# Performance work log

Measured on AMD Instinct MI355X. Metric: run time of the kernel, lower is better.

The kernel has to match this reference:

```python
import jax, jax.numpy as jnp
import numpy as np

EPS = 1e-5

def _lstm_scan(x, mask, Wih, Whh, bih, bhh):
    # x: [B,T,D], mask: [B,T] float (applied to h and c AFTER each step, like the torch code)
    B, T, _ = x.shape
    H = Whh.shape[1]
    x_t = jnp.swapaxes(x, 0, 1)            # [T,B,D]
    m_t = jnp.swapaxes(mask, 0, 1)[:, :, None]  # [T,B,1]
    bias = bih + bhh
    def step(carry, inp):
        h, c = carry
        xt, mt = inp
        gates = xt @ Wih.T + h @ Whh.T + bias   # [B,4H], torch gate order i,f,g,o
        i, f, g, o = jnp.split(gates, 4, axis=-1)
        c = jax.nn.sigmoid(f) * c + jax.nn.sigmoid(i) * jnp.tanh(g)
        h = jax.nn.sigmoid(o) * jnp.tanh(c)
        h = h * mt
        c = c * mt
        return (h, c), h
    h0 = jnp.zeros((B, H), x.dtype)
    _, ys = jax.lax.scan(step, (h0, h0), (x_t, m_t))
    return jnp.swapaxes(ys, 0, 1)          # [B,T,H]

def _layernorm(x, g, b):
    mu = x.mean(-1, keepdims=True)
    var = ((x - mu) ** 2).mean(-1, keepdims=True)
    return (x - mu) * jax.lax.rsqrt(var + EPS) * g + b

def setup_inputs() -> dict:
    key = jax.random.key(0)
    ks = jax.random.split(key, 18)
    B, T, D, H, C = 64, 512, 256, 512, 1000
    def u(k, shape, fan):
        s = 1.0 / np.sqrt(fan)
        return jax.random.uniform(k, shape, jnp.float32, -s, s)
    x = jax.random.normal(ks[0], (B, T, D), jnp.float32)
    reset_mask = jax.random.randint(ks[1], (B, T), 0, 2).astype(jnp.float32)
    return {
        "x": x, "reset_mask": reset_mask,
        # layer 0 LSTM (torch init: U(-1/sqrt(H), 1/sqrt(H)))
        "Wih0": u(ks[2], (4 * H, D), H), "Whh0": u(ks[3], (4 * H, H), H),
        "bih0": u(ks[4], (4 * H,), H), "bhh0": u(ks[5], (4 * H,), H),
        "g0": jnp.ones((H,), jnp.float32), "beta0": jnp.zeros((H,), jnp.float32),
        # layer 1 LSTM
        "Wih1": u(ks[6], (4 * H, H), H), "Whh1": u(ks[7], (4 * H, H), H),
        "bih1": u(ks[8], (4 * H,), H), "bhh1": u(ks[9], (4 * H,), H),
        "g1": jnp.ones((H,), jnp.float32), "beta1": jnp.zeros((H,), jnp.float32),
        # final classifier
        "fcW": u(ks[10], (C, H), H), "fcb": u(ks[11], (C,), H),
    }

def reference(x, reset_mask, Wih0, Whh0, bih0, bhh0, g0, beta0,
              Wih1, Whh1, bih1, bhh1, g1, beta1, fcW, fcb):
    h = _lstm_scan(x, reset_mask, Wih0, Whh0, bih0, bhh0)
    h = _layernorm(jax.nn.relu(h), g0, beta0)
    h = _lstm_scan(h, reset_mask, Wih1, Whh1, bih1, bhh1)
    h = _layernorm(jax.nn.relu(h), g1, beta1)
    return h[:, -1, :] @ fcW.T + fcb        # [B, num_classes]
```

## Files before the change

kernel.cpp:

```cpp
#include <hip/hip_runtime.h>
#include <stdint.h>

#define BB 64
#define TT 512
#define DD 256
#define HH 512
#define NG 2048
#define BT (BB*TT)
#define NCLS 1000
#define MAXS 16

typedef _Float16 f16;
typedef _Float16 f16x2 __attribute__((ext_vector_type(2)));
typedef _Float16 f16x4 __attribute__((ext_vector_type(4)));
typedef _Float16 f16x8 __attribute__((ext_vector_type(8)));
typedef float f32x4 __attribute__((ext_vector_type(4)));

__device__ const int d_OFF[MAXS] = {0,32768,49152,60096,68288,74880,80384,85120,
                                    89216,92864,96192,99200,101952,104512,106880,109120};

__device__ __forceinline__ float sigf(float x) { return 1.0f / (1.0f + __expf(-x)); }
__device__ __forceinline__ float tanh_(float x) {
  float e = __expf(-2.0f * fabsf(x));
  float r = (1.0f - e) / (1.0f + e);
  return copysignf(r, x);
}
__device__ __forceinline__ f32x4 mfma16(f16x8 a, f16x8 b, f32x4 c) {
  return __builtin_amdgcn_mfma_f32_16x16x32_f16(a, b, c, 0, 0, 0);
}
__device__ __forceinline__ void gload16(const void* g, void* l) {
  __builtin_amdgcn_global_load_lds((const __attribute__((address_space(1))) void*)g,
                                   (__attribute__((address_space(3))) void*)l, 16, 0, 0);
}

#define C0 (NG*DD/4)
#define C1 (C0 + NG*HH/4)
#define C2 (C1 + NG*HH/4)
#define C3 (C2 + NG*HH/4)
#define CX (C3 + BT*DD/4)
__global__ __launch_bounds__(256) void prep_weights(
    const float* __restrict__ Wih0, const float* __restrict__ Whh0,
    const float* __restrict__ Wih1, const float* __restrict__ Whh1,
    const float* __restrict__ x,
    const float* __restrict__ bih0, const float* __restrict__ bhh0,
    const float* __restrict__ bih1, const float* __restrict__ bhh1,
    f16* __restrict__ W16ih0, f16* __restrict__ W16hh0,
    f16* __restrict__ W16ih1, f16* __restrict__ W16hh1,
    f16* __restrict__ AX,
    float* __restrict__ bias0, float* __restrict__ bias1) {
  int gi = blockIdx.x * 256 + threadIdx.x;
  for (int i = gi; i < CX; i += gridDim.x * 256) {
    const float* s; f16* d; int o;
    if (i < C0)      { s = Wih0; d = W16ih0; o = i; }
    else if (i < C1) { s = Whh0; d = W16hh0; o = i - C0; }
    else if (i < C2) { s = Wih1; d = W16ih1; o = i - C1; }
    else if (i < C3) { s = Whh1; d = W16hh1; o = i - C2; }
    else             { s = x;    d = AX;     o = i - C3; }
    float4 v = ((const float4*)s)[o];
    f16x4 h = { (f16)v.x, (f16)v.y, (f16)v.z, (f16)v.w };
    ((f16x4*)d)[o] = h;
  }
  if (gi < NG/2) {
    int j = gi * 2;
    bias0[j]   = bih0[j]   + bhh0[j];
    bias0[j+1] = bih0[j+1] + bhh0[j+1];
    bias1[j]   = bih1[j]   + bhh1[j];
    bias1[j+1] = bih1[j+1] + bhh1[j+1];
  }
}

__global__ __launch_bounds__(512) void build_lists(const float* __restrict__ mask,
    int* __restrict__ counts, int* __restrict__ lists,
    int* __restrict__ tailcnt, int* __restrict__ taillist,
    float* __restrict__ selm) {
  int b = blockIdx.x, t = threadIdx.x;
  __shared__ float sm[512];
  __shared__ int lcnt[MAXS], lbase[MAXS];
  sm[t] = mask[b*TT + t];
  if (t < MAXS) lcnt[t] = 0;
  __syncthreads();
  int run = 0;
  for (int j = 1; j <= MAXS; ++j) {
    if (t - j < 0) break;
    if (sm[t - j] != 0.0f) run++; else break;
  }
  selm[b*TT + t] = (run == 0) ? sm[t] : -1.0f;
  bool tail = (run >= MAXS);
  int slot = -1;
  if (!tail && run > 0) slot = atomicAdd(&lcnt[run], 1);
  __syncthreads();
  if (t < MAXS) lbase[t] = atomicAdd(&counts[t*32], lcnt[t]);
  __syncthreads();
  if (!tail && run > 0) lists[d_OFF[run] + lbase[run] + slot] = b*TT + t;
  unsigned long long bal = __ballot(tail);
  int lane = t & 63, w = t >> 6;
  int wpre = __popcll(bal & ((1ull << lane) - 1ull));
  __shared__ int wsum[8];
  if (lane == 0) wsum[w] = __popcll(bal);
  __syncthreads();
  int base = 0;
  for (int i = 0; i < w; ++i) base += wsum[i];
  if (tail) taillist[b*TT + base + wpre] = t;
  if (t == 0) {
    int tot = 0;
    for (int i = 0; i < 8; ++i) tot += wsum[i];
    tailcnt[b] = tot;
  }
}

__global__ __launch_bounds__(512) void proj_act(const f16* __restrict__ A,
    const f16* __restrict__ W, const float* __restrict__ bias,
    f16* __restrict__ G, f16* __restrict__ HS, f16* __restrict__ CS,
    const float* __restrict__ selm, int K) {
  __shared__ __align__(16) f16 smem[128*64 + 256*64];
  f16* As = smem;
  f16* Bs = smem + 128*64;
  __shared__ float sel[128];
  const int nwg = gridDim.x;
  const int cpx = nwg >> 3;
  const int swz = (blockIdx.x & 7) * cpx + (blockIdx.x >> 3);
  const int m0 = (swz >> 3) * 128;
  const int j0 = (swz & 7) * 64;
  const int tid = threadIdx.x;
  const int lane = tid & 63;
  const int w = tid >> 6;
  if (tid < 128) sel[tid] = selm[m0 + tid];

  const f16* asrc[2];
#pragma unroll
  for (int p = 0; p < 2; ++p) {
    int cid = tid + p*512;
    int r = cid >> 3, c = cid & 7;
    int cs = c ^ (r & 7);
    asrc[p] = A + (size_t)(m0 + r)*K + cs*8;
  }
  const f16* bsrc[4];
#pragma unroll
  for (int p = 0; p < 4; ++p) {
    int cid = tid + p*512;
    int grow = cid >> 3, c = cid & 7;
    int cs = c ^ (grow & 7);
    int wrow = (grow >> 6)*512 + j0 + (grow & 63);
    bsrc[p] = W + (size_t)wrow*K + cs*8;
  }

  const int rg = w >> 2;
  const int jg = w & 3;
  const int cl = lane & 15;
  const int kq = lane >> 4;
  f32x4 acc[4][4] = {};

  for (int k0 = 0; k0 < K; k0 += 64) {
#pragma unroll
    for (int p = 0; p < 2; ++p)
      gload16(asrc[p] + k0, As + (tid + p*512)*8);
#pragma unroll
    for (int p = 0; p < 4; ++p)
      gload16(bsrc[p] + k0, Bs + (tid + p*512)*8);
    __syncthreads();
#pragma unroll
    for (int ks = 0; ks < 2; ++ks) {
      int kc = ks*4 + kq;
      f16x8 af[4], bf[4];
#pragma unroll
      for (int mi = 0; mi < 4; ++mi) {
        int row = rg*64 + mi*16 + cl;
        af[mi] = *(const f16x8*)(As + row*64 + ((kc ^ (row & 7))*8));
      }
#pragma unroll
      for (int g = 0; g < 4; ++g) {
        int brow = g*64 + jg*16 + cl;
        bf[g] = *(const f16x8*)(Bs + brow*64 + ((kc ^ (brow & 7))*8));
      }
#pragma unroll
      for (int mi = 0; mi < 4; ++mi)
#pragma unroll
        for (int g = 0; g < 4; ++g)
          acc[mi][g] = mfma16(af[mi], bf[g], acc[mi][g]);
    }
    __syncthreads();
  }

  const int j = j0 + jg*16 + cl;
#pragma unroll
  for (int g = 0; g < 4; ++g) {
    float bb = bias[g*512 + j];
#pragma unroll
    for (int mi = 0; mi < 4; ++mi)
#pragma unroll
      for (int r = 0; r < 4; ++r)
        acc[mi][g][r] += bb;
  }

  f16* stg = smem;
#pragma unroll
  for (int half = 0; half < 2; ++half) {
    if (rg == half) {
#pragma unroll
      for (int mi = 0; mi < 4; ++mi)
#pragma unroll
        for (int g = 0; g < 4; ++g)
#pragma unroll
          for (int r = 0; r < 4; ++r) {
            int row_l = mi*16 + kq*4 + r;
            stg[row_l*264 + g*64 + jg*16 + cl] = (f16)acc[mi][g][r];
          }
    }
    __syncthreads();
    {
      int row_l = tid >> 3, sl = tid & 7;
      int slot = half*64 + row_l;
      int row = m0 + slot;
      int jj = j0 + sl*8;
      f16x8 vi = *(const f16x8*)(stg + row_l*264 +        sl*8);
      f16x8 vf = *(const f16x8*)(stg + row_l*264 +  64 + sl*8);
      f16x8 vg = *(const f16x8*)(stg + row_l*264 + 128 + sl*8);
      f16x8 vo = *(const f16x8*)(stg + row_l*264 + 192 + sl*8);
      float sm = sel[slot];
      if (sm >= 0.0f) {
        f16x8 hv, cv;
#pragma unroll
        for (int e = 0; e < 8; ++e) {
          float c = sigf((float)vi[e]) * tanh_((float)vg[e]);
          float h = sigf((float)vo[e]) * tanh_(c);
          hv[e] = (f16)(h*sm); cv[e] = (f16)(c*sm);
        }
        *(f16x8*)(HS + (size_t)row*HH + jj) = hv;
        *(f16x8*)(CS + (size_t)row*HH + jj) = cv;
      } else {
        *(f16x8*)(G + (size_t)row*NG +        jj) = vi;
        *(f16x8*)(G + (size_t)row*NG +  512 + jj) = vf;
        *(f16x8*)(G + (size_t)row*NG + 1024 + jj) = vg;
        *(f16x8*)(G + (size_t)row*NG + 1536 + jj) = vo;
      }
    }
    __syncthreads();
  }
}

__global__ __launch_bounds__(512) void lstm_step(const f16* __restrict__ Wh,
    const f16* __restrict__ G, f16* __restrict__ HS, f16* __restrict__ CS,
    const float* __restrict__ mask, const int* __restrict__ counts,
    const int* __restrict__ lists, int s) {
  const int cnt = counts[s*32];
  if (cnt == 0) return;
  const int units = ((cnt + 127) >> 7) * 8;
  const int* lst = lists + d_OFF[s];
  const int tid = threadIdx.x;
  const int lane = tid & 63;
  const int w = tid >> 6;
  __shared__ __align__(16) f16 smem[128*64 + 256*64];
  f16* As = smem;
  f16* Bs = smem + 128*64;
  __shared__ int ridx[128];
  __shared__ float rmk[128];
  const int rg = w >> 2;
  const int jg = w & 3;
  const int cl = lane & 15;
  const int kq = lane >> 4;

  for (int u = blockIdx.x; u < units; u += gridDim.x) {
    const int mbase = (u >> 3) * 128;
    const int j0 = (u & 7) * 64;
    if (tid < 128) {
      int i = mbase + tid;
      int r = (i < cnt) ? lst[i] : -1;
      ridx[tid] = r;
      rmk[tid] = (r >= 0) ? mask[r] : 0.0f;
    }
    __syncthreads();

    const f16* asrc[2];
#pragma unroll
    for (int p = 0; p < 2; ++p) {
      int cid = tid + p*512;
      int r = cid >> 3, c = cid & 7;
      int cs = c ^ (r & 7);
      int rr = ridx[r];
      int sr = (rr >= 1 ? rr : 1) - 1;
      asrc[p] = HS + (size_t)sr*HH + cs*8;
    }
    const f16* bsrc[4];
#pragma unroll
    for (int p = 0; p < 4; ++p) {
      int cid = tid + p*512;
      int grow = cid >> 3, c = cid & 7;
      int cs = c ^ (grow & 7);
      int wrow = (grow >> 6)*512 + j0 + (grow & 63);
      bsrc[p] = Wh + (size_t)wrow*HH + cs*8;
    }

    f32x4 acc[4][4] = {};
    for (int k0 = 0; k0 < HH; k0 += 64) {
#pragma unroll
      for (int p = 0; p < 2; ++p)
        gload16(asrc[p] + k0, As + (tid + p*512)*8);
#pragma unroll
      for (int p = 0; p < 4; ++p)
        gload16(bsrc[p] + k0, Bs + (tid + p*512)*8);
      __syncthreads();
#pragma unroll
      for (int ks = 0; ks < 2; ++ks) {
        int kc = ks*4 + kq;
        f16x8 af[4], bf[4];
#pragma unroll
        for (int mi = 0; mi < 4; ++mi) {
          int row = rg*64 + mi*16 + cl;
          af[mi] = *(const f16x8*)(As + row*64 + ((kc ^ (row & 7))*8));
        }
#pragma unroll
        for (int g = 0; g < 4; ++g) {
          int brow = g*64 + jg*16 + cl;
          bf[g] = *(const f16x8*)(Bs + brow*64 + ((kc ^ (brow & 7))*8));
        }
#pragma unroll
        for (int mi = 0; mi < 4; ++mi)
#pragma unroll
          for (int g = 0; g < 4; ++g)
            acc[mi][g] = mfma16(af[mi], bf[g], acc[mi][g]);
      }
      __syncthreads();
    }

    f16* stg = smem;
#pragma unroll
    for (int half = 0; half < 2; ++half) {
      if (rg == half) {
#pragma unroll
        for (int mi = 0; mi < 4; ++mi)
#pragma unroll
          for (int g = 0; g < 4; ++g)
#pragma unroll
            for (int r = 0; r < 4; ++r) {
              int row_l = mi*16 + kq*4 + r;
              stg[row_l*264 + g*64 + jg*16 + cl] = (f16)acc[mi][g][r];
            }
      }
      __syncthreads();
      {
        int row_l = tid >> 3, sl = tid & 7;
        int slot = half*64 + row_l;
        int row = ridx[slot];
        if (row >= 0) {
          int jj = j0 + sl*8;
          f16x8 ai = *(const f16x8*)(stg + row_l*264 +        sl*8);
          f16x8 af2 = *(const f16x8*)(stg + row_l*264 +  64 + sl*8);
          f16x8 ag = *(const f16x8*)(stg + row_l*264 + 128 + sl*8);
          f16x8 ao = *(const f16x8*)(stg + row_l*264 + 192 + sl*8);
          f16x8 Gi = *(const f16x8*)(G + (size_t)row*NG +        jj);
          f16x8 Gf = *(const f16x8*)(G + (size_t)row*NG +  512 + jj);
          f16x8 Gg = *(const f16x8*)(G + (size_t)row*NG + 1024 + jj);
          f16x8 Go = *(const f16x8*)(G + (size_t)row*NG + 1536 + jj);
          f16x8 cp = *(const f16x8*)(CS + (size_t)(row - 1)*HH + jj);
          float m = rmk[slot];
          f16x8 hv, cv;
#pragma unroll
          for (int e = 0; e < 8; ++e) {
            float gi = (float)ai[e] + (float)Gi[e];
            float gf = (float)af2[e] + (float)Gf[e];
            float gg = (float)ag[e] + (float)Gg[e];
            float go = (float)ao[e] + (float)Go[e];
            float c = sigf(gf)*(float)cp[e] + sigf(gi)*tanh_(gg);
            float h = sigf(go)*tanh_(c);
            hv[e] = (f16)(h*m); cv[e] = (f16)(c*m);
          }
          *(f16x8*)(HS + (size_t)row*HH + jj) = hv;
          *(f16x8*)(CS + (size_t)row*HH + jj) = cv;
        }
      }
      __syncthreads();
    }
  }
}

__global__ __launch_bounds__(512) void lstm_step_thin(const f16* __restrict__ Wh,
    const f16* __restrict__ G, f16* __restrict__ HS, f16* __restrict__ CS,
    const float* __restrict__ mask, const int* __restrict__ counts,
    const int* __restrict__ lists, int s) {
  const int cnt = counts[s*32];
  if (cnt == 0) return;
  const int units = ((cnt + 127) >> 7) * 32;
  const int* lst = lists + d_OFF[s];
  const int tid = threadIdx.x;
  const int lane = tid & 63;
  const int w = tid >> 6;
  __shared__ __align__(16) f16 As[128*64];
  __shared__ __align__(16) f16 Bs[64*64];
  __shared__ int ridx[128];
  __shared__ float rmk[128];
  const int cl = lane & 15;
  const int kq = lane >> 4;
  const int rbase = w * 16;

  for (int u = blockIdx.x; u < units; u += gridDim.x) {
    const int mbase = (u >> 5) * 128;
    const int j0 = (u & 31) * 16;
    if (tid < 128) {
      int i = mbase + tid;
      int r = (i < cnt) ? lst[i] : -1;
      ridx[tid] = r;
      rmk[tid] = (r >= 0) ? mask[r] : 0.0f;
    }
    __syncthreads();

    const f16* asrc[2];
#pragma unroll
    for (int p = 0; p < 2; ++p) {
      int cid = tid + p*512;
      int r = cid >> 3, c = cid & 7;
      int cs = c ^ (r & 7);
      int rr = ridx[r];
      int sr = (rr >= 1 ? rr : 1) - 1;
      asrc[p] = HS + (size_t)sr*HH + cs*8;
    }
    const f16* bsrc;
    {
      int grow = tid >> 3, c = tid & 7;
      int cs = c ^ (grow & 7);
      int wrow = (grow >> 4)*512 + j0 + (grow & 15);
      bsrc = Wh + (size_t)wrow*HH + cs*8;
    }

    f32x4 acc[4] = {};
    for (int k0 = 0; k0 < HH; k0 += 64) {
#pragma unroll
      for (int p = 0; p < 2; ++p)
        gload16(asrc[p] + k0, As + (tid + p*512)*8);
      gload16(bsrc + k0, Bs + tid*8);
      __syncthreads();
#pragma unroll
      for (int ks = 0; ks < 2; ++ks) {
        int kc = ks*4 + kq;
        int arow = rbase + cl;
        f16x8 af = *(const f16x8*)(As + arow*64 + ((kc ^ (arow & 7))*8));
        f16x8 bf[4];
#pragma unroll
        for (int g = 0; g < 4; ++g) {
          int brow = g*16 + cl;
          bf[g] = *(const f16x8*)(Bs + brow*64 + ((kc ^ (brow & 7))*8));
        }
#pragma unroll
        for (int g = 0; g < 4; ++g)
          acc[g] = mfma16(af, bf[g], acc[g]);
      }
      __syncthreads();
    }

    const int j = j0 + cl;
#pragma unroll
    for (int r = 0; r < 4; ++r) {
      int slot = rbase + kq*4 + r;
      int row = ridx[slot];
      if (row >= 0) {
        size_t gb = (size_t)row * NG;
        float gi = acc[0][r] + (float)G[gb + j];
        float gf = acc[1][r] + (float)G[gb + 512 + j];
        float gg = acc[2][r] + (float)G[gb + 1024 + j];
        float go = acc[3][r] + (float)G[gb + 1536 + j];
        float cp = (float)CS[(size_t)(row - 1)*HH + j];
        float c = sigf(gf)*cp + sigf(gi)*tanh_(gg);
        float h = sigf(go)*tanh_(c);
        float m = rmk[slot];
        HS[(size_t)row*HH + j] = (f16)(h*m);
        CS[(size_t)row*HH + j] = (f16)(c*m);
      }
    }
    __syncthreads();
  }
}

__global__ __launch_bounds__(512) void lstm_tail(const f16* __restrict__ Wh,
    const f16* __restrict__ G, f16* __restrict__ HS, f16* __restrict__ CS,
    const float* __restrict__ mask, const int* __restrict__ tailcnt,
    const int* __restrict__ taillist) {
  int b = blockIdx.x;
  int n = tailcnt[b];
  if (n == 0) return;
  int tid = threadIdx.x, lane = tid & 63, w = tid >> 6;
  const int rl = lane >> 3;
  const int kb = (lane & 7) * 8;
  __shared__ __align__(16) f16 hsh[HH];
  __shared__ float gsh[NG];
  for (int i = 0; i < n; ++i) {
    int t = taillist[b*TT + i];
    size_t row = (size_t)b*TT + t;
    if (tid < 256)
      ((uint32_t*)hsh)[tid] = ((const uint32_t*)(HS + (row - 1)*HH))[tid];
    __syncthreads();
    f16x8 hreg[8];
#pragma unroll
    for (int kk = 0; kk < 8; ++kk)
      hreg[kk] = *(const f16x8*)(hsh + kb + kk*64);
#pragma unroll 2
    for (int batch = 0; batch < 32; ++batch) {
      int o = (w*32 + batch)*8 + rl;
      const f16* wrow = Wh + (size_t)o*HH + kb;
      float p = 0.0f;
#pragma unroll
      for (int kk = 0; kk < 8; ++kk) {
        f16x8 wv = *(const f16x8*)(wrow + kk*64);
        f16x2 w0 = {wv[0], wv[1]}, w1 = {wv[2], wv[3]}, w2 = {wv[4], wv[5]}, w3 = {wv[6], wv[7]};
        f16x2 h0 = {hreg[kk][0], hreg[kk][1]}, h1 = {hreg[kk][2], hreg[kk][3]},
              h2 = {hreg[kk][4], hreg[kk][5]}, h3 = {hreg[kk][6], hreg[kk][7]};
        p = __builtin_amdgcn_fdot2(w0, h0, p, false);
        p = __builtin_amdgcn_fdot2(w1, h1, p, false);
        p = __builtin_amdgcn_fdot2(w2, h2, p, false);
        p = __builtin_amdgcn_fdot2(w3, h3, p, false);
      }
      p += __shfl_xor(p, 1);
      p += __shfl_xor(p, 2);
      p += __shfl_xor(p, 4);
      if ((lane & 7) == 0) gsh[o] = p + (float)G[row*NG + o];
    }
    __syncthreads();
    {
      float cp = (float)CS[(row - 1)*HH + tid];
      float c = sigf(gsh[512 + tid])*cp + sigf(gsh[tid])*tanh_(gsh[1024 + tid]);
      float h = sigf(gsh[1536 + tid])*tanh_(c);
      float m = mask[row];
      HS[row*HH + tid] = (f16)(h*m);
      CS[row*HH + tid] = (f16)(c*m);
    }
    __syncthreads();
  }
}

__global__ __launch_bounds__(512) void ln_relu(const f16* __restrict__ in,
    const float* __restrict__ g, const float* __restrict__ be,
    f16* __restrict__ out) {
  int lane = threadIdx.x & 63, w = threadIdx.x >> 6;
  int row = blockIdx.x * 8 + w;
  f16x8 hv = *(const f16x8*)(in + (size_t)row*HH + lane*8);
  float xv[8]; float s1 = 0.f, s2 = 0.f;
#pragma unroll
  for (int e = 0; e < 8; ++e) { float x = fmaxf((float)hv[e], 0.f); xv[e] = x; s1 += x; s2 += x*x; }
#pragma unroll
  for (int o = 1; o < 64; o <<= 1) { s1 += __shfl_xor(s1, o); s2 += __shfl_xor(s2, o); }
  float mu = s1 * (1.0f/512.0f);
  float var = s2 * (1.0f/512.0f) - mu*mu;
  float rs = rsqrtf(var + 1e-5f);
  f16x8 ov;
#pragma unroll
  for (int e = 0; e < 8; ++e) ov[e] = (f16)((xv[e] - mu)*rs*g[lane*8+e] + be[lane*8+e]);
  *(f16x8*)(out + (size_t)row*HH + lane*8) = ov;
}

__global__ __launch_bounds__(512) void ln_last(const f16* __restrict__ HS,
    const float* __restrict__ g, const float* __restrict__ be, float* __restrict__ out) {
  int b = blockIdx.x;
  int j = threadIdx.x;
  float x = fmaxf((float)HS[((size_t)b*TT + (TT-1))*HH + j], 0.0f);
  float s1 = x, s2 = x*x;
  for (int o = 32; o > 0; o >>= 1) { s1 += __shfl_down(s1, o); s2 += __shfl_down(s2, o); }
  __shared__ float a1[8], a2[8];
  int w = j >> 6;
  if ((j & 63) == 0) { a1[w] = s1; a2[w] = s2; }
  __syncthreads();
  if (j == 0) {
    float t1 = 0.f, t2 = 0.f;
    for (int i = 0; i < 8; ++i) { t1 += a1[i]; t2 += a2[i]; }
    a1[0] = t1; a2[0] = t2;
  }
  __syncthreads();
  float mu = a1[0] * (1.0f/512.0f);
  float var = a2[0] * (1.0f/512.0f) - mu*mu;
  float y = (x - mu) * rsqrtf(var + 1e-5f) * g[j] + be[j];
  out[b*HH + j] = y;
}

__global__ __launch_bounds__(256) void fc_kernel(const float* __restrict__ hf,
    const float* __restrict__ W, const float* __restrict__ bias, float* __restrict__ out) {
  int b = blockIdx.y;
  int c = blockIdx.x * 256 + threadIdx.x;
  __shared__ float hsh[512];
  hsh[threadIdx.x] = hf[b*HH + threadIdx.x];
  hsh[threadIdx.x + 256] = hf[b*HH + 256 + threadIdx.x];
  __syncthreads();
  if (c < NCLS) {
    const float4* wr = (const float4*)(W + (size_t)c*HH);
    float acc = bias[c];
#pragma unroll 4
    for (int k4 = 0; k4 < 128; ++k4) {
      float4 wv = wr[k4];
      acc += wv.x*hsh[k4*4] + wv.y*hsh[k4*4+1] + wv.z*hsh[k4*4+2] + wv.w*hsh[k4*4+3];
    }
    out[b*NCLS + c] = acc;
  }
}

extern "C" void kernel_launch(void* const* d_in, const int* in_sizes, int n_in,
                              void* d_out, int out_size, void* d_ws, size_t ws_size,
                              hipStream_t stream) {
  (void)in_sizes; (void)n_in; (void)out_size;
  const float* x    = (const float*)d_in[0];
  const float* mask = (const float*)d_in[1];
  const float* Wih0 = (const float*)d_in[2];
  const float* Whh0 = (const float*)d_in[3];
  const float* bih0 = (const float*)d_in[4];
  const float* bhh0 = (const float*)d_in[5];
  const float* g0   = (const float*)d_in[6];
  const float* be0  = (const float*)d_in[7];
  const float* Wih1 = (const float*)d_in[8];
  const float* Whh1 = (const float*)d_in[9];
  const float* bih1 = (const float*)d_in[10];
  const float* bhh1 = (const float*)d_in[11];
  const float* g1   = (const float*)d_in[12];
  const float* be1  = (const float*)d_in[13];
  const float* fcW  = (const float*)d_in[14];
  const float* fcb  = (const float*)d_in[15];
  float* out = (float*)d_out;

  char* ws = (char*)d_ws;
  size_t off = 0;
  auto alloc = [&](size_t bytes) { size_t o = off; off += (bytes + 255) & ~(size_t)255; return o; };
  f16* G      = (f16*)(ws + alloc((size_t)BT*NG*2));
  f16* HS     = (f16*)(ws + alloc((size_t)BT*HH*2));
  f16* CS     = (f16*)(ws + alloc((size_t)BT*HH*2));
  f16* H0LN   = (f16*)(ws + alloc((size_t)BT*HH*2));
  f16* W16ih0 = (f16*)(ws + alloc((size_t)NG*DD*2));
  f16* W16hh0 = (f16*)(ws + alloc((size_t)NG*HH*2));
  f16* W16ih1 = (f16*)(ws + alloc((size_t)NG*HH*2));
  f16* W16hh1 = (f16*)(ws + alloc((size_t)NG*HH*2));
  float* bias0 = (float*)(ws + alloc(NG*4));
  float* bias1 = (float*)(ws + alloc(NG*4));
  int* counts  = (int*)(ws + alloc(4096));
  int* tailcnt = counts + 512;
  int* lists   = (int*)(ws + alloc(111168*4));
  int* taillist= (int*)(ws + alloc((size_t)BT*4));
  float* selm  = (float*)(ws + alloc((size_t)BT*4));
  float* hf    = (float*)(ws + alloc((size_t)BB*HH*4));
  if (ws_size < off) return;

  f16* AX = H0LN;

  hipMemsetAsync(counts, 0, 4096, stream);
  prep_weights<<<dim3(512), dim3(256), 0, stream>>>(Wih0, Whh0, Wih1, Whh1, x,
      bih0, bhh0, bih1, bhh1, W16ih0, W16hh0, W16ih1, W16hh1, AX, bias0, bias1);
  build_lists<<<dim3(BB), dim3(512), 0, stream>>>(mask, counts, lists, tailcnt, taillist, selm);

  for (int layer = 0; layer < 2; ++layer) {
    const f16* Wih16 = layer ? W16ih1 : W16ih0;
    const f16* Whh16 = layer ? W16hh1 : W16hh0;
    const float* bias = layer ? bias1 : bias0;
    const f16* Ain = layer ? H0LN : AX;
    int K = layer ? HH : DD;
    proj_act<<<dim3((BT/128)*8), dim3(512), 0, stream>>>(Ain, Wih16, bias, G, HS, CS, selm, K);
    for (int s = 1; s < 5; ++s)
      lstm_step<<<dim3(512), dim3(512), 0, stream>>>(Whh16, G, HS, CS, mask, counts, lists, s);
    for (int s = 5; s < MAXS; ++s)
      lstm_step_thin<<<dim3(256), dim3(512), 0, stream>>>(Whh16, G, HS, CS, mask, counts, lists, s);
    lstm_tail<<<dim3(BB), dim3(512), 0, stream>>>(Whh16, G, HS, CS, mask, tailcnt, taillist);
    if (layer == 0)
      ln_relu<<<dim3(BT/8), dim3(512), 0, stream>>>(HS, g0, be0, H0LN);
  }

  ln_last<<<dim3(BB), dim3(512), 0, stream>>>(HS, g1, be1, hf);
  fc_kernel<<<dim3(4, BB), dim3(256), 0, stream>>>(hf, fcW, fcb, out);
}
```

Baseline: 804.0 us.

## Double-buffer projection GEMM, fuse head LN+FC, shrink thin step grid

The input-projection GEMM now uses two LDS buffers so the global-to-LDS loads for the next K tile are issued before computing the current one, replacing two barriers per iteration with one. The final layernorm and classifier are merged into a single kernel, which removes one launch and the intermediate buffer. The thin LSTM step kernel now launches with half as many workgroups. Doubling LDS per block may lower occupancy, and the fused head runs only 64 blocks for the FC, which reduces parallelism there.

```diff
diff --git a/kernel.cpp b/kernel.cpp
--- a/kernel.cpp
+++ b/kernel.cpp
@@ -112,10 +112,12 @@
     const f16* __restrict__ W, const float* __restrict__ bias,
     f16* __restrict__ G, f16* __restrict__ HS, f16* __restrict__ CS,
     const float* __restrict__ selm, int K) {
-  __shared__ __align__(16) f16 smem[128*64 + 256*64];
-  f16* As = smem;
-  f16* Bs = smem + 128*64;
+  __shared__ __align__(16) f16 smem[2*128*64 + 2*256*64];
   __shared__ float sel[128];
+  f16* A0 = smem;
+  f16* A1 = smem + 128*64;
+  f16* B0 = smem + 2*128*64;
+  f16* B1 = smem + 2*128*64 + 256*64;
   const int nwg = gridDim.x;
   const int cpx = nwg >> 3;
   const int swz = (blockIdx.x & 7) * cpx + (blockIdx.x >> 3);
@@ -149,15 +151,24 @@
   const int cl = lane & 15;
   const int kq = lane >> 4;
   f32x4 acc[4][4] = {};
-
-  for (int k0 = 0; k0 < K; k0 += 64) {
-#pragma unroll
-    for (int p = 0; p < 2; ++p)
-      gload16(asrc[p] + k0, As + (tid + p*512)*8);
-#pragma unroll
-    for (int p = 0; p < 4; ++p)
-      gload16(bsrc[p] + k0, Bs + (tid + p*512)*8);
-    __syncthreads();
+  const int nt = K >> 6;
+
+#define PSTAGE(Ad, Bd, k0) do { \
+    gload16(asrc[0] + (k0), (Ad) + tid*8); \
+    gload16(asrc[1] + (k0), (Ad) + (tid + 512)*8); \
+    gload16(bsrc[0] + (k0), (Bd) + tid*8); \
+    gload16(bsrc[1] + (k0), (Bd) + (tid + 512)*8); \
+    gload16(bsrc[2] + (k0), (Bd) + (tid + 1024)*8); \
+    gload16(bsrc[3] + (k0), (Bd) + (tid + 1536)*8); \
+  } while (0)
+
+  PSTAGE(A0, B0, 0);
+  asm volatile("s_waitcnt vmcnt(0)" ::: "memory");
+  __builtin_amdgcn_s_barrier();
+
+  f16 *Ac = A0, *Bc = B0, *An = A1, *Bn = B1;
+  for (int t = 0; t < nt; ++t) {
+    if (t + 1 < nt) PSTAGE(An, Bn, (t + 1)*64);
 #pragma unroll
     for (int ks = 0; ks < 2; ++ks) {
       int kc = ks*4 + kq;
@@ -165,12 +176,12 @@
 #pragma unroll
       for (int mi = 0; mi < 4; ++mi) {
         int row = rg*64 + mi*16 + cl;
-        af[mi] = *(const f16x8*)(As + row*64 + ((kc ^ (row & 7))*8));
+        af[mi] = *(const f16x8*)(Ac + row*64 + ((kc ^ (row & 7))*8));
       }
 #pragma unroll
       for (int g = 0; g < 4; ++g) {
         int brow = g*64 + jg*16 + cl;
-        bf[g] = *(const f16x8*)(Bs + brow*64 + ((kc ^ (brow & 7))*8));
+        bf[g] = *(const f16x8*)(Bc + brow*64 + ((kc ^ (brow & 7))*8));
       }
 #pragma unroll
       for (int mi = 0; mi < 4; ++mi)
@@ -178,8 +189,13 @@
         for (int g = 0; g < 4; ++g)
           acc[mi][g] = mfma16(af[mi], bf[g], acc[mi][g]);
     }
-    __syncthreads();
-  }
+    asm volatile("s_waitcnt vmcnt(0)" ::: "memory");
+    __builtin_amdgcn_s_barrier();
+    f16* tp;
+    tp = Ac; Ac = An; An = tp;
+    tp = Bc; Bc = Bn; Bn = tp;
+  }
+#undef PSTAGE
 
   const int j = j0 + jg*16 + cl;
 #pragma unroll
@@ -545,10 +561,12 @@
   *(f16x8*)(out + (size_t)row*HH + lane*8) = ov;
 }
 
-__global__ __launch_bounds__(512) void ln_last(const f16* __restrict__ HS,
-    const float* __restrict__ g, const float* __restrict__ be, float* __restrict__ out) {
+__global__ __launch_bounds__(512) void head_fused(const f16* __restrict__ HS,
+    const float* __restrict__ g, const float* __restrict__ be,
+    const float* __restrict__ W, const float* __restrict__ bias, float* __restrict__ out) {
   int b = blockIdx.x;
   int j = threadIdx.x;
+  __shared__ float hsh[512];
   float x = fmaxf((float)HS[((size_t)b*TT + (TT-1))*HH + j], 0.0f);
   float s1 = x, s2 = x*x;
   for (int o = 32; o > 0; o >>= 1) { s1 += __shfl_down(s1, o); s2 += __shfl_down(s2, o); }
@@ -564,27 +582,21 @@
   __syncthreads();
   float mu = a1[0] * (1.0f/512.0f);
   float var = a2[0] * (1.0f/512.0f) - mu*mu;
-  float y = (x - mu) * rsqrtf(var + 1e-5f) * g[j] + be[j];
-  out[b*HH + j] = y;
-}
-
-__global__ __launch_bounds__(256) void fc_kernel(const float* __restrict__ hf,
-    const float* __restrict__ W, const float* __restrict__ bias, float* __restrict__ out) {
-  int b = blockIdx.y;
-  int c = blockIdx.x * 256 + threadIdx.x;
-  __shared__ float hsh[512];
-  hsh[threadIdx.x] = hf[b*HH + threadIdx.x];
-  hsh[threadIdx.x + 256] = hf[b*HH + 256 + threadIdx.x];
+  hsh[j] = (x - mu) * rsqrtf(var + 1e-5f) * g[j] + be[j];
   __syncthreads();
-  if (c < NCLS) {
-    const float4* wr = (const float4*)(W + (size_t)c*HH);
-    float acc = bias[c];
+#pragma unroll
+  for (int rep = 0; rep < 2; ++rep) {
+    int c = j + rep*512;
+    if (c < NCLS) {
+      const float4* wr = (const float4*)(W + (size_t)c*HH);
+      float acc = bias[c];
 #pragma unroll 4
-    for (int k4 = 0; k4 < 128; ++k4) {
-      float4 wv = wr[k4];
-      acc += wv.x*hsh[k4*4] + wv.y*hsh[k4*4+1] + wv.z*hsh[k4*4+2] + wv.w*hsh[k4*4+3];
-    }
-    out[b*NCLS + c] = acc;
+      for (int k4 = 0; k4 < 128; ++k4) {
+        float4 wv = wr[k4];
+        acc += wv.x*hsh[k4*4] + wv.y*hsh[k4*4+1] + wv.z*hsh[k4*4+2] + wv.w*hsh[k4*4+3];
+      }
+      out[b*NCLS + c] = acc;
+    }
   }
 }
 
@@ -628,7 +640,6 @@
   int* lists   = (int*)(ws + alloc(111168*4));
   int* taillist= (int*)(ws + alloc((size_t)BT*4));
   float* selm  = (float*)(ws + alloc((size_t)BT*4));
-  float* hf    = (float*)(ws + alloc((size_t)BB*HH*4));
   if (ws_size < off) return;
 
   f16* AX = H0LN;
@@ -648,12 +659,11 @@
     for (int s = 1; s < 5; ++s)
       lstm_step<<<dim3(512), dim3(512), 0, stream>>>(Whh16, G, HS, CS, mask, counts, lists, s);
     for (int s = 5; s < MAXS; ++s)
-      lstm_step_thin<<<dim3(256), dim3(512), 0, stream>>>(Whh16, G, HS, CS, mask, counts, lists, s);
+      lstm_step_thin<<<dim3(128), dim3(512), 0, stream>>>(Whh16, G, HS, CS, mask, counts, lists, s);
     lstm_tail<<<dim3(BB), dim3(512), 0, stream>>>(Whh16, G, HS, CS, mask, tailcnt, taillist);
     if (layer == 0)
       ln_relu<<<dim3(BT/8), dim3(512), 0, stream>>>(HS, g0, be0, H0LN);
   }
 
-  ln_last<<<dim3(BB), dim3(512), 0, stream>>>(HS, g1, be1, hf);
-  fc_kernel<<<dim3(4, BB), dim3(256), 0, stream>>>(hf, fcW, fcb, out);
-}
+  head_fused<<<dim3(BB), dim3(512), 0, stream>>>(HS, g1, be1, fcW, fcb, out);
+}
```

Result: slower. 884.0 us (+10.0%).
